# Performance work log

Hardware: AMD Instinct MI355X
Metric: run time of the kernel (lower is better)

## Reference

```python
import jax, jax.numpy as jnp
import numpy as np

N = 100000   # nodes
E = 1600000  # edges
G = 256      # graphs in batch
IN = 128     # in_feats
H = 64       # h_feats


def _xavier(k, shape):
    fan_in, fan_out = shape
    lim = float(np.sqrt(6.0 / (fan_in + fan_out)))
    return jax.random.uniform(k, shape, jnp.float32, -lim, lim)


def setup_inputs() -> dict:
    key = jax.random.key(0)
    ks = jax.random.split(key, 12)
    x = jax.random.normal(ks[0], (N, IN), jnp.float32)
    src = jax.random.randint(ks[1], (E,), 0, N)
    dst = jax.random.randint(ks[2], (E,), 0, N)
    ew = jax.random.uniform(ks[3], (E,), jnp.float32)
    gid = jnp.sort(jax.random.randint(ks[4], (N,), 0, G))
    def lin(k, fi, fo):
        kw, kb = jax.random.split(k)
        lim = float(np.sqrt(1.0 / fi))
        return (jax.random.uniform(kw, (fi, fo), jnp.float32, -lim, lim),
                jax.random.uniform(kb, (fo,), jnp.float32, -lim, lim))
    W1 = _xavier(ks[5], (IN, H)); b1 = jnp.zeros((H,), jnp.float32)
    W2 = _xavier(ks[6], (H, H));  b2 = jnp.zeros((H,), jnp.float32)
    W3 = _xavier(ks[7], (H, H));  b3 = jnp.zeros((H,), jnp.float32)
    Dw1, Db1 = lin(ks[8], H, 16)
    Dw2, Db2 = lin(ks[9], 16, 8)
    Dw3, Db3 = lin(ks[10], 8, 1)
    return {"x": x, "src": src, "dst": dst, "ew": ew, "gid": gid,
            "W1": W1, "b1": b1, "W2": W2, "b2": b2, "W3": W3, "b3": b3,
            "Dw1": Dw1, "Db1": Db1, "Dw2": Dw2, "Db2": Db2, "Dw3": Dw3, "Db3": Db3}


def reference(x, src, dst, ew, gid, W1, b1, W2, b2, W3, b3,
              Dw1, Db1, Dw2, Db2, Dw3, Db3):
    n = x.shape[0]
    # DGL GraphConv norm='both': unweighted degrees, clamped to >= 1
    deg_out = jnp.zeros((n,), x.dtype).at[src].add(1.0)
    deg_in = jnp.zeros((n,), x.dtype).at[dst].add(1.0)
    ns = jax.lax.rsqrt(jnp.maximum(deg_out, 1.0))  # src-side norm
    nd = jax.lax.rsqrt(jnp.maximum(deg_in, 1.0))   # dst-side norm

    def conv(h, W, b):
        # apply weight first (in >= out), then gather-scale-scatter
        h = (h * ns[:, None]) @ W                      # [N, out]
        m = h[src] * ew[:, None]                       # [E, out] edge messages
        agg = jnp.zeros((n, W.shape[1]), h.dtype).at[dst].add(m)
        return agg * nd[:, None] + b

    h = jax.nn.relu(conv(x, W1, b1))
    h = jax.nn.relu(conv(h, W2, b2))
    h = jax.nn.relu(conv(h, W3, b3))

    # mean_nodes: per-graph mean pooling
    counts = jnp.zeros((G,), h.dtype).at[gid].add(1.0)
    pooled = jnp.zeros((G, h.shape[1]), h.dtype).at[gid].add(h)
    pooled = pooled / jnp.maximum(counts, 1.0)[:, None]

    h = jax.nn.relu(pooled @ Dw1 + Db1)
    h = jax.nn.relu(h @ Dw2 + Db2)
    return jax.nn.sigmoid(h @ Dw3 + Db3)  # [G, 1]
```

## Files before the change

kernel.cpp:

```cpp
#include <hip/hip_runtime.h>
#include <math.h>

#define N_NODES 100000
#define N_EDGES 1600000
#define G_GRAPHS 256
#define IN_F 128
#define H_F 64

#define HB 40
#define HCHUNK (N_EDGES / HB)
#define NWORDS (N_NODES / 4)
#define HNODES 25000
#define HWORDS (HNODES / 4)
#define HR 4

#define NREG 160
#define REG_NODES 625
#define BUCKET_CAP 11000
#define BSPAN 6400
#define NB_BUCKET (N_EDGES / BSPAN)

typedef unsigned int uint_t;
typedef unsigned short ushort_t;
typedef unsigned char uchar_t;
typedef __attribute__((ext_vector_type(8))) short short8;
typedef __attribute__((ext_vector_type(4))) float floatx4;
typedef __attribute__((ext_vector_type(2))) float floatx2;

__device__ __forceinline__ ushort_t f2bf(float f) {
  uint_t u = __float_as_uint(f);
  uint_t r = (u + 0x7fffu + ((u >> 16) & 1u)) >> 16;
  return (ushort_t)r;
}
__device__ __forceinline__ float bflo(uint_t u) { return __uint_as_float(u << 16); }
__device__ __forceinline__ uchar_t f2fp8(float f) {
  return (uchar_t)(__builtin_amdgcn_cvt_pk_fp8_f32(f, f, 0, false) & 0xff);
}

__global__ __launch_bounds__(256) void build_a_kernel(
    const int* __restrict__ src, const int* __restrict__ dst,
    const float* __restrict__ ew, int* __restrict__ bcnt,
    uint2* __restrict__ bucket, uint_t* __restrict__ p8src) {
  __shared__ uint_t shm[BSPAN + 2 * NREG];
  if (blockIdx.x < NB_BUCKET) {
    uint_t* rl = shm;
    int* cnt = (int*)(shm + BSPAN);
    int* cur = cnt + NREG;
    const int e0 = blockIdx.x * BSPAN;

    for (int i = threadIdx.x; i < NREG; i += 256) cnt[i] = 0;
    __syncthreads();

    for (int i = threadIdx.x; i < BSPAN; i += 256) {
      uint_t d = (uint_t)dst[e0 + i];
      uint_t r = d / REG_NODES;
      uint_t loc = d - r * REG_NODES;
      rl[i] = (r << 16) | loc;
      atomicAdd(&cnt[r], 1);
    }
    __syncthreads();

    for (int i = threadIdx.x; i < NREG; i += 256)
      cur[i] = atomicAdd(&bcnt[i], cnt[i]);
    __syncthreads();

    for (int i = threadIdx.x; i < BSPAN; i += 256) {
      uint_t v = rl[i];
      uint_t r = v >> 16, loc = v & 0xffffu;
      int pos = atomicAdd(&cur[r], 1);
      if (pos < BUCKET_CAP)
        bucket[(size_t)r * BUCKET_CAP + pos] = make_uint2(
            (loc << 17) | (uint_t)src[e0 + i], __float_as_uint(ew[e0 + i]));
    }
  } else {
    uint_t* h = shm;
    const int idx = blockIdx.x - NB_BUCKET;
    const int r = idx / HB;
    const int b = idx % HB;
    const uint_t rbase = (uint_t)(r * HNODES);

    for (int i = threadIdx.x; i < HWORDS; i += 256) h[i] = 0u;
    __syncthreads();

    const uint4* k4 = (const uint4*)(src + b * HCHUNK);
    for (int i = threadIdx.x; i < HCHUNK / 4; i += 256) {
      uint4 v = k4[i];
      uint_t t;
      t = v.x - rbase; if (t < (uint_t)HNODES) atomicAdd(&h[t >> 2], 1u << ((t & 3u) * 8u));
      t = v.y - rbase; if (t < (uint_t)HNODES) atomicAdd(&h[t >> 2], 1u << ((t & 3u) * 8u));
      t = v.z - rbase; if (t < (uint_t)HNODES) atomicAdd(&h[t >> 2], 1u << ((t & 3u) * 8u));
      t = v.w - rbase; if (t < (uint_t)HNODES) atomicAdd(&h[t >> 2], 1u << ((t & 3u) * 8u));
    }
    __syncthreads();

    uint_t* outp = p8src + (size_t)b * NWORDS + r * HWORDS;
    for (int i = threadIdx.x; i < HWORDS; i += 256) outp[i] = h[i];
  }
}

__global__ __launch_bounds__(256) void build_b_kernel(
    const uint2* __restrict__ bucket, const int* __restrict__ bcnt,
    const uint_t* __restrict__ p8src, uint_t* __restrict__ csr,
    int2* __restrict__ rc, float* __restrict__ nd, float* __restrict__ ns) {
  __shared__ uint_t staged[BUCKET_CAP];
  __shared__ int cnt[REG_NODES];
  __shared__ int sc[REG_NODES];
  __shared__ int ts[256];
  const int tid = threadIdx.x;
  if (blockIdx.x >= NREG) {
    int w = (blockIdx.x - NREG) * 256 + tid;
    if (w >= NWORDS) return;
    int c0 = 0, c1 = 0, c2 = 0, c3 = 0;
    for (int b = 0; b < HB; ++b) {
      uint_t xv = p8src[(size_t)b * NWORDS + w];
      c0 += (int)(xv & 0xffu);
      c1 += (int)((xv >> 8) & 0xffu);
      c2 += (int)((xv >> 16) & 0xffu);
      c3 += (int)((xv >> 24) & 0xffu);
    }
    ((float4*)ns)[w] = make_float4(
        rsqrtf(fmaxf((float)c0, 1.0f)), rsqrtf(fmaxf((float)c1, 1.0f)),
        rsqrtf(fmaxf((float)c2, 1.0f)), rsqrtf(fmaxf((float)c3, 1.0f)));
    return;
  }
  const int r = blockIdx.x;
  const int nE = min(bcnt[r], BUCKET_CAP);

  ts[tid] = (tid < NREG) ? min(bcnt[tid], BUCKET_CAP) : 0;
  for (int i = tid; i < REG_NODES; i += 256) cnt[i] = 0;
  __syncthreads();
  for (int off = 1; off < 256; off <<= 1) {
    int t = (tid >= off) ? ts[tid - off] : 0;
    __syncthreads();
    ts[tid] += t;
    __syncthreads();
  }
  const int csr_base = (r == 0) ? 0 : ts[r - 1];
  __syncthreads();

  const uint2* bk = bucket + (size_t)r * BUCKET_CAP;
  for (int i = tid; i < nE; i += 256) atomicAdd(&cnt[bk[i].x >> 17], 1);
  __syncthreads();

  const int loc0 = tid * 3;
  int c3v[3], s = 0;
#pragma unroll
  for (int k = 0; k < 3; ++k) {
    int idx = loc0 + k;
    c3v[k] = (idx < REG_NODES) ? cnt[idx] : 0;
    s += c3v[k];
  }
  __syncthreads();
  ts[tid] = s;
  __syncthreads();
  for (int off = 1; off < 256; off <<= 1) {
    int t = (tid >= off) ? ts[tid - off] : 0;
    __syncthreads();
    ts[tid] += t;
    __syncthreads();
  }
  int run = (tid == 0) ? 0 : ts[tid - 1];
#pragma unroll
  for (int k = 0; k < 3; ++k) {
    int idx = loc0 + k;
    if (idx < REG_NODES) {
      sc[idx] = run;
      int v = r * REG_NODES + idx;
      rc[v] = make_int2(csr_base + run, c3v[k]);
      nd[v] = rsqrtf(fmaxf((float)c3v[k], 1.0f));
      run += c3v[k];
    }
  }
  __syncthreads();

  for (int i = tid; i < nE; i += 256) {
    uint2 e = bk[i];
    uint_t loc = e.x >> 17;
    int pos = atomicAdd(&sc[loc], 1);
    staged[pos] = ((uint_t)(f2bf(__uint_as_float(e.y)) & 0x7fff) << 17) |
                  (e.x & 0x1ffffu);
  }
  __syncthreads();

  for (int i = tid; i < nE; i += 256) csr[csr_base + i] = staged[i];
}

template <int K, bool AFP32>
__global__ __launch_bounds__(256) void gemm_mfma_kernel(
    const void* __restrict__ Xin, const float* __restrict__ W,
    const float* __restrict__ ns, uchar_t* __restrict__ T, int ntiles) {
  constexpr int CH = K / 32;
  constexpr int WROW = K + 8;
  __shared__ __align__(16) ushort_t Wt[64 * WROW];
  const int tid = threadIdx.x;

  for (int i = tid; i < K * 64; i += 256) {
    int k = i >> 6, nn = i & 63;
    Wt[nn * WROW + k] = f2bf(W[i]);
  }
  __syncthreads();

  const int wave = tid >> 6;
  const int lane = tid & 63;
  const int tile = blockIdx.x * 4 + wave;
  if (tile >= ntiles) return;
  const int m = lane & 15;
  const int q = lane >> 4;
  const int node0 = tile * 16;

  short8 afrag[CH];
  if (AFP32) {
    const float* xr = (const float*)Xin + (size_t)(node0 + m) * K + q * 8;
#pragma unroll
    for (int c = 0; c < CH; ++c) {
      float4 xa = *(const float4*)(xr + c * 32);
      float4 xb = *(const float4*)(xr + c * 32 + 4);
      short8 a;
      a[0] = (short)f2bf(xa.x); a[1] = (short)f2bf(xa.y);
      a[2] = (short)f2bf(xa.z); a[3] = (short)f2bf(xa.w);
      a[4] = (short)f2bf(xb.x); a[5] = (short)f2bf(xb.y);
      a[6] = (short)f2bf(xb.z); a[7] = (short)f2bf(xb.w);
      afrag[c] = a;
    }
  } else {
    const ushort_t* xr = (const ushort_t*)Xin + (size_t)(node0 + m) * K + q * 8;
#pragma unroll
    for (int c = 0; c < CH; ++c)
      afrag[c] = *(const short8*)(xr + c * 32);
  }

  floatx4 acc[4];
#pragma unroll
  for (int t = 0; t < 4; ++t) acc[t] = (floatx4){0.f, 0.f, 0.f, 0.f};

#pragma unroll
  for (int t = 0; t < 4; ++t) {
    const ushort_t* wr = &Wt[(t * 16 + m) * WROW + q * 8];
#pragma unroll
    for (int c = 0; c < CH; ++c) {
      short8 bfrag = *(const short8*)(wr + c * 32);
      acc[t] = __builtin_amdgcn_mfma_f32_16x16x32_bf16(afrag[c], bfrag, acc[t], 0, 0, 0);
    }
  }

  float4 nsv = *(const float4*)(ns + node0 + q * 4);
  const float nsa[4] = {nsv.x, nsv.y, nsv.z, nsv.w};
#pragma unroll
  for (int t = 0; t < 4; ++t) {
#pragma unroll
    for (int r = 0; r < 4; ++r) {
      int node = node0 + q * 4 + r;
      T[(size_t)node * 64 + t * 16 + m] = f2fp8(acc[t][r] * nsa[r]);
    }
  }
}

#define GACC(p, w)                                                   \
  a = __builtin_amdgcn_cvt_pk_f32_fp8((p).x, false);                 \
  acc[0] = fmaf(a.x, (w), acc[0]); acc[1] = fmaf(a.y, (w), acc[1]);  \
  a = __builtin_amdgcn_cvt_pk_f32_fp8((p).x, true);                  \
  acc[2] = fmaf(a.x, (w), acc[2]); acc[3] = fmaf(a.y, (w), acc[3]);  \
  a = __builtin_amdgcn_cvt_pk_f32_fp8((p).y, false);                 \
  acc[4] = fmaf(a.x, (w), acc[4]); acc[5] = fmaf(a.y, (w), acc[5]);  \
  a = __builtin_amdgcn_cvt_pk_f32_fp8((p).y, true);                  \
  acc[6] = fmaf(a.x, (w), acc[6]); acc[7] = fmaf(a.y, (w), acc[7]);

__global__ __launch_bounds__(256) void gather_kernel(
    const uint_t* __restrict__ csr, const int2* __restrict__ rc,
    const uchar_t* __restrict__ T, const float* __restrict__ nd,
    const float* __restrict__ b, ushort_t* __restrict__ H, int n) {
  int id = blockIdx.x * blockDim.x + threadIdx.x;
  const int lane = threadIdx.x & 63;
  const int o = lane >> 3, l = lane & 7;
  int v = (id >> 6) * 8 + o;
  if (v >= n) return;
  int2 rcv = rc[v];
  const int start = rcv.x, cnt = rcv.y;

  float acc[8] = {0, 0, 0, 0, 0, 0, 0, 0};
  floatx2 a;
  int k = 0;
  for (; k + 3 < cnt; k += 4) {
    uint_t e1 = csr[start + k];
    uint_t e2 = csr[start + k + 1];
    uint_t e3 = csr[start + k + 2];
    uint_t e4 = csr[start + k + 3];
    uint2 p1 = *((const uint2*)(T + (size_t)(e1 & 0x1ffffu) * 64) + l);
    uint2 p2 = *((const uint2*)(T + (size_t)(e2 & 0x1ffffu) * 64) + l);
    uint2 p3 = *((const uint2*)(T + (size_t)(e3 & 0x1ffffu) * 64) + l);
    uint2 p4 = *((const uint2*)(T + (size_t)(e4 & 0x1ffffu) * 64) + l);
    float w1 = __uint_as_float((e1 >> 17) << 16);
    float w2 = __uint_as_float((e2 >> 17) << 16);
    float w3 = __uint_as_float((e3 >> 17) << 16);
    float w4 = __uint_as_float((e4 >> 17) << 16);
    GACC(p1, w1)
    GACC(p2, w2)
    GACC(p3, w3)
    GACC(p4, w4)
  }
  for (; k < cnt; ++k) {
    uint_t e1 = csr[start + k];
    float w1 = __uint_as_float((e1 >> 17) << 16);
    uint2 p1 = *((const uint2*)(T + (size_t)(e1 & 0x1ffffu) * 64) + l);
    GACC(p1, w1)
  }

  const float ndv = nd[v];
  float4 b0 = *(const float4*)&b[l * 8];
  float4 b1 = *(const float4*)&b[l * 8 + 4];
  uint4 ov;
  ov.x = (uint_t)f2bf(fmaxf(fmaf(acc[0], ndv, b0.x), 0.f)) |
         ((uint_t)f2bf(fmaxf(fmaf(acc[1], ndv, b0.y), 0.f)) << 16);
  ov.y = (uint_t)f2bf(fmaxf(fmaf(acc[2], ndv, b0.z), 0.f)) |
         ((uint_t)f2bf(fmaxf(fmaf(acc[3], ndv, b0.w), 0.f)) << 16);
  ov.z = (uint_t)f2bf(fmaxf(fmaf(acc[4], ndv, b1.x), 0.f)) |
         ((uint_t)f2bf(fmaxf(fmaf(acc[5], ndv, b1.y), 0.f)) << 16);
  ov.w = (uint_t)f2bf(fmaxf(fmaf(acc[6], ndv, b1.z), 0.f)) |
         ((uint_t)f2bf(fmaxf(fmaf(acc[7], ndv, b1.w), 0.f)) << 16);
  *((uint4*)(H + (size_t)v * 64) + l) = ov;
}

__global__ __launch_bounds__(256) void pool_mlp_kernel(
    const ushort_t* __restrict__ H, const int* __restrict__ gid,
    const float* __restrict__ Dw1, const float* __restrict__ Db1,
    const float* __restrict__ Dw2, const float* __restrict__ Db2,
    const float* __restrict__ Dw3, const float* __restrict__ Db3,
    float* __restrict__ out) {
  __shared__ float red[4][64];
  __shared__ float mean[64];
  __shared__ float h1s[16], h2s[8];
  const int g = blockIdx.x;
  int l = 0, r = N_NODES;
  while (l < r) { int m = (l + r) >> 1; if (gid[m] < g) l = m + 1; else r = m; }
  const int lo = l;
  r = N_NODES;
  while (l < r) { int m = (l + r) >> 1; if (gid[m] < g + 1) l = m + 1; else r = m; }
  const int hi = l;

  const int j = threadIdx.x & 63, s = threadIdx.x >> 6;
  float acc = 0.0f;
  for (int node = lo + s; node < hi; node += 4)
    acc += bflo((uint_t)H[(size_t)node * 64 + j]);
  red[s][j] = acc;
  __syncthreads();
  if (threadIdx.x < 64) {
    float inv = 1.0f / fmaxf((float)(hi - lo), 1.0f);
    mean[j] = (red[0][j] + red[1][j] + red[2][j] + red[3][j]) * inv;
  }
  __syncthreads();
  if (threadIdx.x < 16) {
    int o = threadIdx.x;
    float a = Db1[o];
#pragma unroll
    for (int k = 0; k < 64; ++k) a = fmaf(mean[k], Dw1[k * 16 + o], a);
    h1s[o] = fmaxf(a, 0.0f);
  }
  __syncthreads();
  if (threadIdx.x < 8) {
    int o = threadIdx.x;
    float a = Db2[o];
#pragma unroll
    for (int k = 0; k < 16; ++k) a = fmaf(h1s[k], Dw2[k * 8 + o], a);
    h2s[o] = fmaxf(a, 0.0f);
  }
  __syncthreads();
  if (threadIdx.x == 0) {
    float a = Db3[0];
#pragma unroll
    for (int k = 0; k < 8; ++k) a = fmaf(h2s[k], Dw3[k], a);
    out[g] = 1.0f / (1.0f + expf(-a));
  }
}

extern "C" void kernel_launch(void* const* d_in, const int* in_sizes, int n_in,
                              void* d_out, int out_size, void* d_ws, size_t ws_size,
                              hipStream_t stream) {
  const float* x   = (const float*)d_in[0];
  const int*   src = (const int*)  d_in[1];
  const int*   dst = (const int*)  d_in[2];
  const float* ew  = (const float*)d_in[3];
  const int*   gid = (const int*)  d_in[4];
  const float* W1  = (const float*)d_in[5];
  const float* b1  = (const float*)d_in[6];
  const float* W2  = (const float*)d_in[7];
  const float* b2  = (const float*)d_in[8];
  const float* W3  = (const float*)d_in[9];
  const float* b3  = (const float*)d_in[10];
  const float* Dw1 = (const float*)d_in[11];
  const float* Db1 = (const float*)d_in[12];
  const float* Dw2 = (const float*)d_in[13];
  const float* Db2 = (const float*)d_in[14];
  const float* Dw3 = (const float*)d_in[15];
  const float* Db3 = (const float*)d_in[16];
  float* out = (float*)d_out;

  char* ws = (char*)d_ws;
  uchar_t*  T8    = (uchar_t*)ws;
  ushort_t* Hb    = (ushort_t*)(T8 + (size_t)N_NODES * 64);
  uint_t*   csr   = (uint_t*)(Hb + (size_t)N_NODES * 64);
  uint_t*   p8src = (uint_t*)(csr + N_EDGES);
  float*    ns    = (float*)(p8src + (size_t)HB * NWORDS);
  float*    nd    = ns + N_NODES;
  int2*     rc    = (int2*)(nd + N_NODES);
  int*      bcnt  = (int*)(rc + N_NODES);
  uint2*    bucket = (uint2*)T8;

  const int NTILES  = N_NODES / 16;
  const int NB_A    = NB_BUCKET + HR * HB;
  const int NB_B    = NREG + (NWORDS + 255) / 256;
  const int NB_GEMM = (NTILES + 3) / 4;
  const int NB_GATH = (N_NODES * 8 + 255) / 256;

  hipMemsetAsync(bcnt, 0, NREG * sizeof(int), stream);
  build_a_kernel<<<NB_A, 256, 0, stream>>>(src, dst, ew, bcnt, bucket, p8src);
  build_b_kernel<<<NB_B, 256, 0, stream>>>(bucket, bcnt, p8src, csr, rc, nd, ns);

  gemm_mfma_kernel<IN_F, true><<<NB_GEMM, 256, 0, stream>>>(x, W1, ns, T8, NTILES);
  gather_kernel<<<NB_GATH, 256, 0, stream>>>(csr, rc, T8, nd, b1, Hb, N_NODES);
  gemm_mfma_kernel<H_F, false><<<NB_GEMM, 256, 0, stream>>>(Hb, W2, ns, T8, NTILES);
  gather_kernel<<<NB_GATH, 256, 0, stream>>>(csr, rc, T8, nd, b2, Hb, N_NODES);
  gemm_mfma_kernel<H_F, false><<<NB_GEMM, 256, 0, stream>>>(Hb, W3, ns, T8, NTILES);
  gather_kernel<<<NB_GATH, 256, 0, stream>>>(csr, rc, T8, nd, b3, Hb, N_NODES);

  pool_mlp_kernel<<<G_GRAPHS, 256, 0, stream>>>(Hb, gid, Dw1, Db1, Dw2, Db2,
                                                Dw3, Db3, out);
}
```

Baseline: 302.1 us.

## Fuse gather with next-layer GEMM and fold mean pooling into last gather

New measurement: 295.4 us. -2.2%, faster.

```diff
diff --git a/kernel.cpp b/kernel.cpp
--- a/kernel.cpp
+++ b/kernel.cpp
@@ -265,68 +265,187 @@
   a = __builtin_amdgcn_cvt_pk_f32_fp8((p).y, true);                  \
   acc[6] = fmaf(a.x, (w), acc[6]); acc[7] = fmaf(a.y, (w), acc[7]);
 
-__global__ __launch_bounds__(256) void gather_kernel(
+template <bool POOL>
+__global__ __launch_bounds__(256) void fused_kernel(
     const uint_t* __restrict__ csr, const int2* __restrict__ rc,
     const uchar_t* __restrict__ T, const float* __restrict__ nd,
-    const float* __restrict__ b, ushort_t* __restrict__ H, int n) {
-  int id = blockIdx.x * blockDim.x + threadIdx.x;
-  const int lane = threadIdx.x & 63;
+    const float* __restrict__ bias, const float* __restrict__ ns,
+    const float* __restrict__ W, uchar_t* __restrict__ Tout,
+    const int* __restrict__ gid, float* __restrict__ pooled) {
+  constexpr int WROW = H_F + 8;
+  __shared__ __align__(16) ushort_t Hs[64 * WROW];
+  __shared__ __align__(16) ushort_t Wt[64 * WROW];
+  __shared__ float gaccF[4 * 64];
+  __shared__ int g0s;
+  const int tid = threadIdx.x;
+  const int node_base = blockIdx.x * 64;
+
+  if constexpr (POOL) {
+    gaccF[tid] = 0.0f;
+    if (tid == 0) g0s = gid[node_base];
+  } else {
+    for (int i = tid; i < H_F * 64; i += 256) {
+      int k = i >> 6, nn = i & 63;
+      Wt[nn * WROW + k] = f2bf(W[i]);
+    }
+  }
+  __syncthreads();
+
+  const int lane = tid & 63;
+  const int wv = tid >> 6;
   const int o = lane >> 3, l = lane & 7;
-  int v = (id >> 6) * 8 + o;
-  if (v >= n) return;
-  int2 rcv = rc[v];
-  const int start = rcv.x, cnt = rcv.y;
-
-  float acc[8] = {0, 0, 0, 0, 0, 0, 0, 0};
-  floatx2 a;
-  int k = 0;
-  for (; k + 3 < cnt; k += 4) {
-    uint_t e1 = csr[start + k];
-    uint_t e2 = csr[start + k + 1];
-    uint_t e3 = csr[start + k + 2];
-    uint_t e4 = csr[start + k + 3];
-    uint2 p1 = *((const uint2*)(T + (size_t)(e1 & 0x1ffffu) * 64) + l);
-    uint2 p2 = *((const uint2*)(T + (size_t)(e2 & 0x1ffffu) * 64) + l);
-    uint2 p3 = *((const uint2*)(T + (size_t)(e3 & 0x1ffffu) * 64) + l);
-    uint2 p4 = *((const uint2*)(T + (size_t)(e4 & 0x1ffffu) * 64) + l);
-    float w1 = __uint_as_float((e1 >> 17) << 16);
-    float w2 = __uint_as_float((e2 >> 17) << 16);
-    float w3 = __uint_as_float((e3 >> 17) << 16);
-    float w4 = __uint_as_float((e4 >> 17) << 16);
-    GACC(p1, w1)
-    GACC(p2, w2)
-    GACC(p3, w3)
-    GACC(p4, w4)
-  }
-  for (; k < cnt; ++k) {
-    uint_t e1 = csr[start + k];
-    float w1 = __uint_as_float((e1 >> 17) << 16);
-    uint2 p1 = *((const uint2*)(T + (size_t)(e1 & 0x1ffffu) * 64) + l);
-    GACC(p1, w1)
-  }
-
-  const float ndv = nd[v];
-  float4 b0 = *(const float4*)&b[l * 8];
-  float4 b1 = *(const float4*)&b[l * 8 + 4];
-  uint4 ov;
-  ov.x = (uint_t)f2bf(fmaxf(fmaf(acc[0], ndv, b0.x), 0.f)) |
-         ((uint_t)f2bf(fmaxf(fmaf(acc[1], ndv, b0.y), 0.f)) << 16);
-  ov.y = (uint_t)f2bf(fmaxf(fmaf(acc[2], ndv, b0.z), 0.f)) |
-         ((uint_t)f2bf(fmaxf(fmaf(acc[3], ndv, b0.w), 0.f)) << 16);
-  ov.z = (uint_t)f2bf(fmaxf(fmaf(acc[4], ndv, b1.x), 0.f)) |
-         ((uint_t)f2bf(fmaxf(fmaf(acc[5], ndv, b1.y), 0.f)) << 16);
-  ov.w = (uint_t)f2bf(fmaxf(fmaf(acc[6], ndv, b1.z), 0.f)) |
-         ((uint_t)f2bf(fmaxf(fmaf(acc[7], ndv, b1.w), 0.f)) << 16);
-  *((uint4*)(H + (size_t)v * 64) + l) = ov;
+
+#pragma unroll 1
+  for (int pass = 0; pass < 2; ++pass) {
+    const int ln = pass * 32 + wv * 8 + o;
+    const int v = node_base + ln;
+    if (v < N_NODES) {
+      int2 rcv = rc[v];
+      const int start = rcv.x, cnt = rcv.y;
+      float acc[8] = {0, 0, 0, 0, 0, 0, 0, 0};
+      floatx2 a;
+      int k = 0;
+      for (; k + 7 < cnt; k += 8) {
+        uint_t e1 = csr[start + k];
+        uint_t e2 = csr[start + k + 1];
+        uint_t e3 = csr[start + k + 2];
+        uint_t e4 = csr[start + k + 3];
+        uint_t e5 = csr[start + k + 4];
+        uint_t e6 = csr[start + k + 5];
+        uint_t e7 = csr[start + k + 6];
+        uint_t e8 = csr[start + k + 7];
+        uint2 p1 = *((const uint2*)(T + (size_t)(e1 & 0x1ffffu) * 64) + l);
+        uint2 p2 = *((const uint2*)(T + (size_t)(e2 & 0x1ffffu) * 64) + l);
+        uint2 p3 = *((const uint2*)(T + (size_t)(e3 & 0x1ffffu) * 64) + l);
+        uint2 p4 = *((const uint2*)(T + (size_t)(e4 & 0x1ffffu) * 64) + l);
+        uint2 p5 = *((const uint2*)(T + (size_t)(e5 & 0x1ffffu) * 64) + l);
+        uint2 p6 = *((const uint2*)(T + (size_t)(e6 & 0x1ffffu) * 64) + l);
+        uint2 p7 = *((const uint2*)(T + (size_t)(e7 & 0x1ffffu) * 64) + l);
+        uint2 p8 = *((const uint2*)(T + (size_t)(e8 & 0x1ffffu) * 64) + l);
+        float w1 = __uint_as_float((e1 >> 17) << 16);
+        float w2 = __uint_as_float((e2 >> 17) << 16);
+        float w3 = __uint_as_float((e3 >> 17) << 16);
+        float w4 = __uint_as_float((e4 >> 17) << 16);
+        float w5 = __uint_as_float((e5 >> 17) << 16);
+        float w6 = __uint_as_float((e6 >> 17) << 16);
+        float w7 = __uint_as_float((e7 >> 17) << 16);
+        float w8 = __uint_as_float((e8 >> 17) << 16);
+        GACC(p1, w1) GACC(p2, w2) GACC(p3, w3) GACC(p4, w4)
+        GACC(p5, w5) GACC(p6, w6) GACC(p7, w7) GACC(p8, w8)
+      }
+      for (; k + 3 < cnt; k += 4) {
+        uint_t e1 = csr[start + k];
+        uint_t e2 = csr[start + k + 1];
+        uint_t e3 = csr[start + k + 2];
+        uint_t e4 = csr[start + k + 3];
+        uint2 p1 = *((const uint2*)(T + (size_t)(e1 & 0x1ffffu) * 64) + l);
+        uint2 p2 = *((const uint2*)(T + (size_t)(e2 & 0x1ffffu) * 64) + l);
+        uint2 p3 = *((const uint2*)(T + (size_t)(e3 & 0x1ffffu) * 64) + l);
+        uint2 p4 = *((const uint2*)(T + (size_t)(e4 & 0x1ffffu) * 64) + l);
+        float w1 = __uint_as_float((e1 >> 17) << 16);
+        float w2 = __uint_as_float((e2 >> 17) << 16);
+        float w3 = __uint_as_float((e3 >> 17) << 16);
+        float w4 = __uint_as_float((e4 >> 17) << 16);
+        GACC(p1, w1) GACC(p2, w2) GACC(p3, w3) GACC(p4, w4)
+      }
+      for (; k < cnt; ++k) {
+        uint_t e1 = csr[start + k];
+        float w1 = __uint_as_float((e1 >> 17) << 16);
+        uint2 p1 = *((const uint2*)(T + (size_t)(e1 & 0x1ffffu) * 64) + l);
+        GACC(p1, w1)
+      }
+
+      const float ndv = nd[v];
+      float4 b0 = *(const float4*)&bias[l * 8];
+      float4 b1v = *(const float4*)&bias[l * 8 + 4];
+      if constexpr (!POOL) {
+        uint4 ov;
+        ov.x = (uint_t)f2bf(fmaxf(fmaf(acc[0], ndv, b0.x), 0.f)) |
+               ((uint_t)f2bf(fmaxf(fmaf(acc[1], ndv, b0.y), 0.f)) << 16);
+        ov.y = (uint_t)f2bf(fmaxf(fmaf(acc[2], ndv, b0.z), 0.f)) |
+               ((uint_t)f2bf(fmaxf(fmaf(acc[3], ndv, b0.w), 0.f)) << 16);
+        ov.z = (uint_t)f2bf(fmaxf(fmaf(acc[4], ndv, b1v.x), 0.f)) |
+               ((uint_t)f2bf(fmaxf(fmaf(acc[5], ndv, b1v.y), 0.f)) << 16);
+        ov.w = (uint_t)f2bf(fmaxf(fmaf(acc[6], ndv, b1v.z), 0.f)) |
+               ((uint_t)f2bf(fmaxf(fmaf(acc[7], ndv, b1v.w), 0.f)) << 16);
+        *((uint4*)&Hs[ln * WROW + l * 8]) = ov;
+      } else {
+        const float bb[8] = {b0.x, b0.y, b0.z, b0.w, b1v.x, b1v.y, b1v.z, b1v.w};
+        float vals[8];
+#pragma unroll
+        for (int f = 0; f < 8; ++f)
+          vals[f] = bflo((uint_t)f2bf(fmaxf(fmaf(acc[f], ndv, bb[f]), 0.f)));
+        int g = gid[v];
+        int gl = g - g0s;
+        if (gl >= 0 && gl < 4) {
+#pragma unroll
+          for (int f = 0; f < 8; ++f)
+            atomicAdd(&gaccF[gl * 64 + l * 8 + f], vals[f]);
+        } else {
+#pragma unroll
+          for (int f = 0; f < 8; ++f)
+            atomicAdd(&pooled[(size_t)g * 64 + l * 8 + f], vals[f]);
+        }
+      }
+    }
+  }
+  __syncthreads();
+
+  if constexpr (!POOL) {
+    const int m = lane & 15, q = lane >> 4;
+    const int node0 = node_base + wv * 16;
+    if (node0 < N_NODES) {
+      short8 afrag[2];
+      const ushort_t* xr = &Hs[(wv * 16 + m) * WROW + q * 8];
+      afrag[0] = *(const short8*)(xr);
+      afrag[1] = *(const short8*)(xr + 32);
+
+      floatx4 acc4[4];
+#pragma unroll
+      for (int t = 0; t < 4; ++t) acc4[t] = (floatx4){0.f, 0.f, 0.f, 0.f};
+#pragma unroll
+      for (int t = 0; t < 4; ++t) {
+        const ushort_t* wr = &Wt[(t * 16 + m) * WROW + q * 8];
+#pragma unroll
+        for (int c = 0; c < 2; ++c) {
+          short8 bfrag = *(const short8*)(wr + c * 32);
+          acc4[t] = __builtin_amdgcn_mfma_f32_16x16x32_bf16(afrag[c], bfrag,
+                                                           acc4[t], 0, 0, 0);
+        }
+      }
+      float4 nsv = *(const float4*)(ns + node0 + q * 4);
+      const float nsa[4] = {nsv.x, nsv.y, nsv.z, nsv.w};
+#pragma unroll
+      for (int t = 0; t < 4; ++t) {
+#pragma unroll
+        for (int r2 = 0; r2 < 4; ++r2) {
+          int node = node0 + q * 4 + r2;
+          Tout[(size_t)node * 64 + t * 16 + m] = f2fp8(acc4[t][r2] * nsa[r2]);
+        }
+      }
+    }
+  } else {
+    int vlast = node_base + 63;
+    if (vlast >= N_NODES) vlast = N_NODES - 1;
+    int span = gid[vlast] - g0s + 1;
+    if (span > 4) span = 4;
+    if (tid < span * 64) {
+      int gl = tid >> 6, j = tid & 63;
+      int g = g0s + gl;
+      if (g < G_GRAPHS) {
+        float vsum = gaccF[gl * 64 + j];
+        if (vsum != 0.0f) atomicAdd(&pooled[(size_t)g * 64 + j], vsum);
+      }
+    }
+  }
 }
 
 __global__ __launch_bounds__(256) void pool_mlp_kernel(
-    const ushort_t* __restrict__ H, const int* __restrict__ gid,
+    const float* __restrict__ pooled, const int* __restrict__ gid,
     const float* __restrict__ Dw1, const float* __restrict__ Db1,
     const float* __restrict__ Dw2, const float* __restrict__ Db2,
     const float* __restrict__ Dw3, const float* __restrict__ Db3,
     float* __restrict__ out) {
-  __shared__ float red[4][64];
   __shared__ float mean[64];
   __shared__ float h1s[16], h2s[8];
   const int g = blockIdx.x;
@@ -337,15 +456,9 @@
   while (l < r) { int m = (l + r) >> 1; if (gid[m] < g + 1) l = m + 1; else r = m; }
   const int hi = l;
 
-  const int j = threadIdx.x & 63, s = threadIdx.x >> 6;
-  float acc = 0.0f;
-  for (int node = lo + s; node < hi; node += 4)
-    acc += bflo((uint_t)H[(size_t)node * 64 + j]);
-  red[s][j] = acc;
-  __syncthreads();
   if (threadIdx.x < 64) {
     float inv = 1.0f / fmaxf((float)(hi - lo), 1.0f);
-    mean[j] = (red[0][j] + red[1][j] + red[2][j] + red[3][j]) * inv;
+    mean[threadIdx.x] = pooled[(size_t)g * 64 + threadIdx.x] * inv;
   }
   __syncthreads();
   if (threadIdx.x < 16) {
@@ -395,33 +508,39 @@
   float* out = (float*)d_out;
 
   char* ws = (char*)d_ws;
-  uchar_t*  T8    = (uchar_t*)ws;
-  ushort_t* Hb    = (ushort_t*)(T8 + (size_t)N_NODES * 64);
-  uint_t*   csr   = (uint_t*)(Hb + (size_t)N_NODES * 64);
-  uint_t*   p8src = (uint_t*)(csr + N_EDGES);
-  float*    ns    = (float*)(p8src + (size_t)HB * NWORDS);
-  float*    nd    = ns + N_NODES;
-  int2*     rc    = (int2*)(nd + N_NODES);
-  int*      bcnt  = (int*)(rc + N_NODES);
-  uint2*    bucket = (uint2*)T8;
+  const size_t TSZ = (size_t)N_NODES * 64;
+  const size_t BUCKET_BYTES = (size_t)NREG * BUCKET_CAP * 8;
+  uchar_t*  T_a   = (uchar_t*)ws;
+  uchar_t*  T_b   = (uchar_t*)(ws + TSZ);
+  uint2*    bucket = (uint2*)ws;
+  char* p = ws + BUCKET_BYTES;
+  uint_t*   csr   = (uint_t*)p;          p += (size_t)N_EDGES * 4;
+  uint_t*   p8src = (uint_t*)p;          p += (size_t)HB * NWORDS * 4;
+  float*    ns    = (float*)p;           p += (size_t)N_NODES * 4;
+  float*    nd    = (float*)p;           p += (size_t)N_NODES * 4;
+  int2*     rc    = (int2*)p;            p += (size_t)N_NODES * 8;
+  int*      bcnt  = (int*)p;             p += (size_t)NREG * 4;
+  float*    pooled = (float*)p;
 
   const int NTILES  = N_NODES / 16;
   const int NB_A    = NB_BUCKET + HR * HB;
   const int NB_B    = NREG + (NWORDS + 255) / 256;
   const int NB_GEMM = (NTILES + 3) / 4;
-  const int NB_GATH = (N_NODES * 8 + 255) / 256;
-
-  hipMemsetAsync(bcnt, 0, NREG * sizeof(int), stream);
+  const int NB_F    = (N_NODES + 63) / 64;
+
+  hipMemsetAsync(bcnt, 0,
+                 NREG * sizeof(int) + G_GRAPHS * H_F * sizeof(float), stream);
   build_a_kernel<<<NB_A, 256, 0, stream>>>(src, dst, ew, bcnt, bucket, p8src);
   build_b_kernel<<<NB_B, 256, 0, stream>>>(bucket, bcnt, p8src, csr, rc, nd, ns);
 
-  gemm_mfma_kernel<IN_F, true><<<NB_GEMM, 256, 0, stream>>>(x, W1, ns, T8, NTILES);
-  gather_kernel<<<NB_GATH, 256, 0, stream>>>(csr, rc, T8, nd, b1, Hb, N_NODES);
-  gemm_mfma_kernel<H_F, false><<<NB_GEMM, 256, 0, stream>>>(Hb, W2, ns, T8, NTILES);
-  gather_kernel<<<NB_GATH, 256, 0, stream>>>(csr, rc, T8, nd, b2, Hb, N_NODES);
-  gemm_mfma_kernel<H_F, false><<<NB_GEMM, 256, 0, stream>>>(Hb, W3, ns, T8, NTILES);
-  gather_kernel<<<NB_GATH, 256, 0, stream>>>(csr, rc, T8, nd, b3, Hb, N_NODES);
-
-  pool_mlp_kernel<<<G_GRAPHS, 256, 0, stream>>>(Hb, gid, Dw1, Db1, Dw2, Db2,
+  gemm_mfma_kernel<IN_F, true><<<NB_GEMM, 256, 0, stream>>>(x, W1, ns, T_a, NTILES);
+  fused_kernel<false><<<NB_F, 256, 0, stream>>>(csr, rc, T_a, nd, b1, ns, W2,
+                                                T_b, nullptr, nullptr);
+  fused_kernel<false><<<NB_F, 256, 0, stream>>>(csr, rc, T_b, nd, b2, ns, W3,
+                                                T_a, nullptr, nullptr);
+  fused_kernel<true><<<NB_F, 256, 0, stream>>>(csr, rc, T_a, nd, b3, nullptr,
+                                               nullptr, nullptr, gid, pooled);
+
+  pool_mlp_kernel<<<G_GRAPHS, 256, 0, stream>>>(pooled, gid, Dw1, Db1, Dw2, Db2,
                                                 Dw3, Db3, out);
 }
```
